# Performance work log

Measured on AMD Instinct MI355X. Metric: run time of the kernel, lower is better.

The kernel has to match this reference:

```python
import jax, jax.numpy as jnp
import numpy as np
from jax import lax

N_VAR, BATCH, N_IN, N_OUT, N_FEAT, T = 4, 32, 32, 32, 32, 256
EPS, COUPLING, GMAX, GMIN = 0.05, 0.2, 10.0, 0.01
DT, RMIN, RMAX, CMIN, CMAX = 0.1, 1e5, 1e7, 1e-7, 1e-4
ETA = np.array([0.05, 0.5, 0.3, 3.0], dtype=np.float32)  # printed-tanh activation params


def _init_theta(key, n_in, n_out):
    # xavier_uniform -> min-max normalize to [0,1], then bias-column construction as in pLayer.__init__
    a = float(np.sqrt(6.0 / (n_in + 2 + n_out)))
    t = jax.random.uniform(key, (n_in + 2, n_out), minval=-a, maxval=a)
    t = (t - t.min()) / (t.max() - t.min())
    t = t.at[-1, :].add(GMAX)
    t = t.at[-2, :].set(ETA[2] / (1.0 - ETA[2]) * (t[:-2].sum(0) + t[-1]))
    return t.astype(jnp.float32)


def setup_inputs():
    key = jax.random.key(0)
    kx, k1, k2 = jax.random.split(key, 3)
    x = jax.random.uniform(kx, (N_VAR, BATCH, N_IN, T), dtype=jnp.float32)
    theta1_ = _init_theta(k1, N_IN, N_OUT)
    theta2_ = _init_theta(k2, N_OUT * (N_FEAT + 1), N_OUT)
    # LearnableFilter init from beta_init (C_ fixed at -10, R_ is logit of normalized R)
    betas = np.linspace(0.1, 0.9, N_OUT)
    b0 = betas[:N_FEAT]
    b1 = betas[::-1][:N_FEAT]
    C_mean = 1.0 / (1.0 + np.exp(10.0)) * (CMAX - CMIN) + CMIN
    def r_(b):
        R_true = b * DT / (1.0 - b) / C_mean
        Rn = (R_true - RMIN) / (RMAX - RMIN)
        return np.log(Rn / (1.0 - Rn))
    Rlf_ = jnp.asarray(np.broadcast_to(np.stack([r_(b0), r_(b1)], -1), (N_OUT, N_FEAT, 2)).copy(), dtype=jnp.float32)
    Clf_ = jnp.full((N_OUT, N_FEAT, 2), -10.0, dtype=jnp.float32)
    return {"x": x, "theta1_": theta1_, "theta2_": theta2_, "Rlf_": Rlf_, "Clf_": Clf_}


def _theta_eff(theta_):
    # clamp + magnitude pruning with straight-through estimator
    t = jnp.clip(theta_, -GMAX, GMAX)
    t = jnp.where(jnp.abs(t) < GMIN, 0.0, t)
    return lax.stop_gradient(t) + theta_ - lax.stop_gradient(theta_)


def _pmac(a, theta_, key):
    # a: [N,B,Cin,T] -> [N,B,Cout,T]; printed MAC with sign-split weights and ideal inverter INV(a)=-a
    th = _theta_eff(theta_)
    noise = (jax.random.uniform(key, (N_VAR,) + th.shape) * 2.0 - 1.0) * EPS + 1.0
    thn = th[None] * noise  # [N,M,O]
    W = jnp.abs(thn) / (jnp.sum(jnp.abs(thn), axis=1, keepdims=True) + 1e-10)
    pos = (thn >= 0).astype(a.dtype)
    neg = 1.0 - pos
    ar = jnp.swapaxes(a, 2, 3)  # [N,B,T,Cin]
    ones = jnp.ones(ar.shape[:-1] + (1,), a.dtype)
    a_ext = jnp.concatenate([ar, ones, jnp.zeros_like(ones)], axis=-1)  # [N,B,T,M]
    a_neg = (-a_ext).at[..., -1].set(0.0)  # INV(a_ext) with last column zeroed
    z = jnp.einsum('nbtm,nmo->nbto', a_ext, W * pos) + jnp.einsum('nbtm,nmo->nbto', a_neg, W * neg)
    act = ETA[0] + ETA[1] * jnp.tanh((z - ETA[2]) * ETA[3])
    return jnp.swapaxes(act, 2, 3)


def _filter_bank(x, R_, C_, key):
    # x: [K,N,B,T]; first-order leaky integrator with fresh per-step R/C/mu noise, random init state
    K, N, B, Tt = x.shape
    Rt = jax.nn.sigmoid(R_) * (RMAX - RMIN) + RMIN  # [K]
    Ct = jax.nn.sigmoid(C_) * (CMAX - CMIN) + CMIN
    kR, kC, kmu, k0 = jax.random.split(key, 4)
    nR = (jax.random.uniform(kR, (Tt, K, N, 1)) * 2.0 - 1.0) * EPS + 1.0
    nC = (jax.random.uniform(kC, (Tt, K, N, 1)) * 2.0 - 1.0) * EPS + 1.0
    mu = jax.random.uniform(kmu, (Tt, K, N, 1)) * COUPLING + 1.0
    RC = mu * (Rt[None, :, None, None] * nR) * (Ct[None, :, None, None] * nC)
    beta = RC / (RC + DT)  # [T,K,N,1]
    s0 = jax.random.uniform(k0, (K, N, B))  # random_state=True
    xs = jnp.moveaxis(x, 3, 0)  # [T,K,N,B]
    def step(s, inp):
        x_t, b_t = inp
        return b_t * s + (1.0 - b_t) * x_t, s  # emit pre-update state (torch keeps init, drops last)
    _, outs = lax.scan(step, s0, (xs, beta))
    return jnp.moveaxis(outs, 0, 3)  # [K,N,B,T]


def reference(x, theta1_, theta2_, Rlf_, Clf_):
    key = jax.random.key(42)
    k1, k2, k3, k4 = jax.random.split(key, 4)
    a1 = _pmac(x, theta1_, k1)  # [N,B,C,T]
    N, B, C, Tt = a1.shape
    F = N_FEAT
    K = C * F
    xc = jnp.transpose(a1, (2, 0, 1, 3))  # [C,N,B,T]
    xk = jnp.broadcast_to(xc[:, None], (C, F, N, B, Tt)).reshape(K, N, B, Tt)
    y = _filter_bank(xk, Rlf_[..., 0].reshape(K), Clf_[..., 0].reshape(K), k2)
    y = _filter_bank(y, Rlf_[..., 1].reshape(K), Clf_[..., 1].reshape(K), k3)
    y = y.reshape(C, F, N, B, Tt)
    feats = jnp.concatenate([xc[:, None], y], axis=1)  # [C,F+1,N,B,T]
    h = jnp.transpose(feats, (2, 3, 0, 1, 4)).reshape(N, B, C * (F + 1), Tt)
    return _pmac(h, theta2_, k4)  # [N,B,N_out,T]
```

## Files before the change

kernel.cpp:

```cpp
#include <hip/hip_runtime.h>
#include <stdint.h>

#define C_RMIN 100000.0f
#define C_RMAX 10000000.0f
#define C_CMIN 1e-07f
#define C_CMAX 1e-04f
#define C_DT   0.1f
#define C_EPS  0.05f
#define C_COUP 0.2f

typedef __attribute__((ext_vector_type(8))) short bf16x8;
typedef __attribute__((ext_vector_type(4))) float floatx4;

__host__ __device__ inline void tf2x32(uint32_t k0, uint32_t k1,
                                       uint32_t& x0, uint32_t& x1) {
  uint32_t ks2 = k0 ^ k1 ^ 0x1BD11BDAu;
  uint32_t a = x0 + k0, b = x1 + k1;
#define TFR(r) a += b; b = (b << (r)) | (b >> (32 - (r))); b ^= a;
  TFR(13) TFR(15) TFR(26) TFR(6)
  a += k1;  b += ks2 + 1u;
  TFR(17) TFR(29) TFR(16) TFR(24)
  a += ks2; b += k0 + 2u;
  TFR(13) TFR(15) TFR(26) TFR(6)
  a += k0;  b += k1 + 3u;
  TFR(17) TFR(29) TFR(16) TFR(24)
  a += k1;  b += ks2 + 4u;
  TFR(13) TFR(15) TFR(26) TFR(6)
  a += ks2; b += k0 + 5u;
#undef TFR
  x0 = a; x1 = b;
}

__device__ inline float unif01(uint32_t k0, uint32_t k1, uint32_t e) {
  uint32_t x0 = 0u, x1 = e;
  tf2x32(k0, k1, x0, x1);
  uint32_t bits = x0 ^ x1;
  return __uint_as_float((bits >> 9) | 0x3F800000u) - 1.0f;
}

__device__ inline float theta_eff(float t) {
  t = fminf(fmaxf(t, -10.0f), 10.0f);
  return (fabsf(t) < 0.01f) ? 0.0f : t;
}

__device__ inline float sigmoidf(float x) { return 1.0f / (1.0f + expf(-x)); }

__device__ inline float noise_mul(float u) { return (u * 2.0f - 1.0f) * C_EPS + 1.0f; }

__global__ __launch_bounds__(256) void prep_kernel(
    const float* __restrict__ Rlf, const float* __restrict__ Clf,
    const float* __restrict__ theta1, const float* __restrict__ theta2,
    const float* __restrict__ x,
    float* __restrict__ beta12, float* __restrict__ a1,
    float* __restrict__ denom2p,
    uint32_t k1a, uint32_t k1b, uint32_t k4a, uint32_t k4b,
    uint32_t kR1a, uint32_t kR1b, uint32_t kC1a, uint32_t kC1b,
    uint32_t kM1a, uint32_t kM1b,
    uint32_t kR2a, uint32_t kR2b, uint32_t kC2a, uint32_t kC2b,
    uint32_t kM2a, uint32_t kM2b) {
  __shared__ float red[256];
  __shared__ float vsm[34 * 32];
  __shared__ float S1s[33 * 32];
  __shared__ float xs[32][256];
  int bid = blockIdx.x;
  int tid = threadIdx.x;
  if (bid < 32) {
    int n = bid >> 3, p = bid & 7;
    int o = tid & 31;
    int jc = tid >> 5;
    int j0 = p * 8 + jc;
    float part = 0.0f;
    for (int j = j0; j < 1058; j += 64) {
      float t = theta_eff(theta2[j * 32 + o]);
      float u = unif01(k4a, k4b, (uint32_t)((n * 1058 + j) * 32 + o));
      part += fabsf(t * noise_mul(u));
    }
    red[jc * 32 + o] = part;
    __syncthreads();
    if (jc == 0) {
      float s = 0.0f;
      for (int q = 0; q < 8; ++q) s += red[q * 32 + o];
      denom2p[(n * 8 + p) * 32 + o] = s;
    }
  } else if (bid < 160) {
    int blk = bid - 32;
    int n = blk >> 5, b = blk & 31;
    int o = tid & 31, mq = tid >> 5;
    float dp = 0.0f;
    for (int m = mq; m < 34; m += 8) {
      float t = theta_eff(theta1[m * 32 + o]);
      float v = t * noise_mul(unif01(k1a, k1b, (uint32_t)((n * 34 + m) * 32 + o)));
      vsm[m * 32 + o] = v;
      dp += fabsf(v);
    }
    red[mq * 32 + o] = dp;
    const float* xp = x + (size_t)((n * 32 + b) * 32) * 256;
    __syncthreads();
    for (int idx = tid; idx < 33 * 32; idx += 256) {
      int oo = idx & 31;
      float den = 1e-10f;
#pragma unroll
      for (int q = 0; q < 8; ++q) den += red[q * 32 + oo];
      S1s[idx] = vsm[idx] / den;
    }
    for (int m = 0; m < 32; ++m) xs[m][tid] = xp[m * 256 + tid];
    __syncthreads();
    float* ap = a1 + (size_t)((n * 32 + b) * 32) * 256;
    int t = tid;
    for (int oo = 0; oo < 32; ++oo) {
      float z = S1s[32 * 32 + oo];
#pragma unroll
      for (int m = 0; m < 32; ++m) z += xs[m][t] * S1s[m * 32 + oo];
      ap[oo * 256 + t] = 0.05f + 0.5f * tanhf((z - 0.3f) * 3.0f);
    }
  } else {
    int u = (bid - 160) * 256 + tid;
    int k = u & 1023;
    int tc = (u >> 10) & 31;
    int n = u >> 15;
    float Rt1 = sigmoidf(Rlf[k * 2 + 0]) * (C_RMAX - C_RMIN) + C_RMIN;
    float Ct1 = sigmoidf(Clf[k * 2 + 0]) * (C_CMAX - C_CMIN) + C_CMIN;
    float Rt2 = sigmoidf(Rlf[k * 2 + 1]) * (C_RMAX - C_RMIN) + C_RMIN;
    float Ct2 = sigmoidf(Clf[k * 2 + 1]) * (C_CMAX - C_CMIN) + C_CMIN;
#pragma unroll
    for (int it = 0; it < 8; ++it) {
      int t = tc * 8 + it;
      uint32_t e = (uint32_t)((t * 1024 + k) * 4 + n);
      float nR1 = noise_mul(unif01(kR1a, kR1b, e));
      float nC1 = noise_mul(unif01(kC1a, kC1b, e));
      float mu1 = unif01(kM1a, kM1b, e) * C_COUP + 1.0f;
      float rc1 = mu1 * (Rt1 * nR1) * (Ct1 * nC1);
      float nR2 = noise_mul(unif01(kR2a, kR2b, e));
      float nC2 = noise_mul(unif01(kC2a, kC2b, e));
      float mu2 = unif01(kM2a, kM2b, e) * C_COUP + 1.0f;
      float rc2 = mu2 * (Rt2 * nR2) * (Ct2 * nC2);
      float2 bb = { rc1 / (rc1 + C_DT), rc2 / (rc2 + C_DT) };
      *(float2*)&beta12[(size_t)(((n * 256 + t) * 1024) + k) * 2] = bb;
    }
  }
}

#define YP 264
#define YPLANE (16 * YP)

__global__ __launch_bounds__(320) void fk6_kernel(
    const float* __restrict__ a1, const float* __restrict__ theta2,
    const float* __restrict__ denom2p,
    const float* __restrict__ beta12, float* __restrict__ zpart,
    uint32_t k01a, uint32_t k01b, uint32_t k02a, uint32_t k02b,
    uint32_t k4a, uint32_t k4b) {
  int bid = blockIdx.x;
  int qr = bid & 3;
  int nb = bid >> 2;
  int n = nb >> 5, b = nb & 31;
  int tid = threadIdx.x;

  __shared__ __align__(16) uint8_t smem[50176];
  uint16_t* yh = (uint16_t*)smem;
  uint16_t* yl = (uint16_t*)(smem + 16896);
  short*    wf = (short*)(smem + 33792);
  __shared__ float sden[32];

  const float* a1nb = a1 + (size_t)nb * 8192;
  const float* bp = beta12 + ((size_t)n * 262144 + qr * 256) * 2;
  float* zout = zpart + (size_t)bid * 8192;

  if (tid < 32) {
    float d = 1e-10f;
#pragma unroll
    for (int q = 0; q < 8; ++q) d += denom2p[(n * 8 + q) * 32 + tid];
    sden[tid] = d;
  }
  __syncthreads();

  float s1 = 0.0f, s2 = 0.0f;
  int cc = 0;

  if (tid < 256) {
    int k = qr * 256 + tid;
    uint32_t e0 = (uint32_t)((k * 4 + n) * 32 + b);
    s1 = unif01(k01a, k01b, e0);
    s2 = unif01(k02a, k02b, e0);
    cc = k >> 5;
    for (int it = 0; it < 32; ++it) {
      int widx = it * 256 + tid;
      int j = widx & 7;
      int lane_ = (widx >> 3) & 63;
      int ot = (widx >> 9) & 1;
      int ks = widx >> 10;
      int sub = ((lane_ >> 4) << 3) + j;
      int jrow = (qr * 8 + ks) * 33 + 1 + sub;
      int oo = ot * 16 + (lane_ & 15);
      float th = theta_eff(theta2[jrow * 32 + oo]);
      float u = unif01(k4a, k4b, (uint32_t)((n * 1058 + jrow) * 32 + oo));
      float w = th * noise_mul(u) / sden[oo];
      uint32_t wb = __float_as_uint(w);
      uint32_t hi = (wb + 0x7FFFu + ((wb >> 16) & 1u)) >> 16;
      wf[(ks * 2 + ot) * 512 + lane_ * 8 + j] = (short)(uint16_t)hi;
    }
  }
  __syncthreads();

  for (int c = 0; c <= 16; ++c) {
    if (tid < 256) {
      if (c < 16) {
        uint16_t* yhb = yh + (c & 1) * YPLANE;
        uint16_t* ylb = yl + (c & 1) * YPLANE;
        int t0 = c * 16;
#pragma unroll
        for (int it = 0; it < 16; ++it) {
          int t = t0 + it;
          uint32_t sb = __float_as_uint(s2);
          uint32_t hi = sb >> 16;
          float fhi = __uint_as_float(sb & 0xFFFF0000u);
          uint32_t lo = __float_as_uint(s2 - fhi) >> 16;
          yhb[it * YP + tid] = (uint16_t)hi;
          ylb[it * YP + tid] = (uint16_t)lo;
          float2 bb = *(const float2*)&bp[(size_t)(t * 1024 + tid) * 2];
          float xv = a1nb[cc * 256 + t];
          s2 = bb.y * s2 + (1.0f - bb.y) * s1;
          s1 = bb.x * s1 + (1.0f - bb.x) * xv;
        }
      }
    } else if (c >= 1) {
      int lane = tid - 256;
      int tc = lane & 15, q = lane >> 4;
      const uint16_t* yhr = yh + ((c - 1) & 1) * YPLANE + tc * YP + q * 8;
      const uint16_t* ylr = yl + ((c - 1) & 1) * YPLANE + tc * YP + q * 8;
      floatx4 acc0a = {0,0,0,0}, acc0b = {0,0,0,0};
      floatx4 acc1a = {0,0,0,0}, acc1b = {0,0,0,0};
#pragma unroll
      for (int ks = 0; ks < 8; ++ks) {
        bf16x8 ah = *(const bf16x8*)(yhr + ks * 32);
        bf16x8 al = *(const bf16x8*)(ylr + ks * 32);
        bf16x8 bh0 = *(const bf16x8*)&wf[(ks * 2 + 0) * 512 + lane * 8];
        bf16x8 bh1 = *(const bf16x8*)&wf[(ks * 2 + 1) * 512 + lane * 8];
        if (ks & 1) {
          acc0b = __builtin_amdgcn_mfma_f32_16x16x32_bf16(ah, bh0, acc0b, 0, 0, 0);
          acc0b = __builtin_amdgcn_mfma_f32_16x16x32_bf16(al, bh0, acc0b, 0, 0, 0);
          acc1b = __builtin_amdgcn_mfma_f32_16x16x32_bf16(ah, bh1, acc1b, 0, 0, 0);
          acc1b = __builtin_amdgcn_mfma_f32_16x16x32_bf16(al, bh1, acc1b, 0, 0, 0);
        } else {
          acc0a = __builtin_amdgcn_mfma_f32_16x16x32_bf16(ah, bh0, acc0a, 0, 0, 0);
          acc0a = __builtin_amdgcn_mfma_f32_16x16x32_bf16(al, bh0, acc0a, 0, 0, 0);
          acc1a = __builtin_amdgcn_mfma_f32_16x16x32_bf16(ah, bh1, acc1a, 0, 0, 0);
          acc1a = __builtin_amdgcn_mfma_f32_16x16x32_bf16(al, bh1, acc1a, 0, 0, 0);
        }
      }
      int t0 = (c - 1) * 16;
      floatx4 r0 = acc0a + acc0b;
      floatx4 r1 = acc1a + acc1b;
      *(floatx4*)&zout[tc * 256 + t0 + q * 4] = r0;
      *(floatx4*)&zout[(16 + tc) * 256 + t0 + q * 4] = r1;
    }
    __syncthreads();
  }
}

__global__ __launch_bounds__(256) void cb2_kernel(
    const float* __restrict__ a1, const float* __restrict__ theta2,
    const float* __restrict__ denom2p,
    const float* __restrict__ zpart, float* __restrict__ out,
    uint32_t k4a, uint32_t k4b) {
  int nb = blockIdx.x;
  int n = nb >> 5;
  int t = threadIdx.x;
  __shared__ float xs[32][256];
  __shared__ float wd[33 * 32];
  __shared__ float sden[32];
  if (t < 32) {
    float d = 1e-10f;
#pragma unroll
    for (int q = 0; q < 8; ++q) d += denom2p[(n * 8 + q) * 32 + t];
    sden[t] = d;
  }
  const float* a1nb = a1 + (size_t)nb * 8192;
  for (int c = 0; c < 32; ++c) xs[c][t] = a1nb[c * 256 + t];
  __syncthreads();
  for (int idx = t; idx < 33 * 32; idx += 256) {
    int r = idx >> 5, oo = idx & 31;
    int j = (r < 32) ? r * 33 : 1056;
    float th = theta_eff(theta2[j * 32 + oo]);
    float u = unif01(k4a, k4b, (uint32_t)((n * 1058 + j) * 32 + oo));
    wd[idx] = th * noise_mul(u) / sden[oo];
  }
  __syncthreads();
  const float* zp = zpart + (size_t)nb * 4 * 8192;
  float* op = out + (size_t)nb * 8192;
  for (int o = 0; o < 32; ++o) {
    float z = wd[32 * 32 + o];
#pragma unroll
    for (int c = 0; c < 32; ++c) z += xs[c][t] * wd[c * 32 + o];
    z += zp[o * 256 + t] + zp[8192 + o * 256 + t] +
         zp[16384 + o * 256 + t] + zp[24576 + o * 256 + t];
    op[o * 256 + t] = 0.05f + 0.5f * tanhf((z - 0.3f) * 3.0f);
  }
}

struct KeyPair { uint32_t a, b; };

static inline void split4_host(KeyPair key, KeyPair out[4]) {
  for (uint32_t i = 0; i < 4; ++i) {
    uint32_t x0 = 0u, x1 = i;
    tf2x32(key.a, key.b, x0, x1);
    out[i] = {x0, x1};
  }
}

extern "C" void kernel_launch(void* const* d_in, const int* in_sizes, int n_in,
                              void* d_out, int out_size, void* d_ws, size_t ws_size,
                              hipStream_t stream) {
  const float* x   = (const float*)d_in[0];
  const float* th1 = (const float*)d_in[1];
  const float* th2 = (const float*)d_in[2];
  const float* Rlf = (const float*)d_in[3];
  const float* Clf = (const float*)d_in[4];
  float* out = (float*)d_out;
  float* ws = (float*)d_ws;

  float* den2p  = ws;
  float* a1     = ws + 1024;
  float* beta12 = ws + 1049600;
  float* zpart  = ws + 3146752;

  KeyPair root{0u, 42u};
  KeyPair kk[4];  split4_host(root, kk);
  KeyPair f1[4];  split4_host(kk[1], f1);
  KeyPair f2[4];  split4_host(kk[2], f2);

  prep_kernel<<<dim3(672), dim3(256), 0, stream>>>(
      Rlf, Clf, th1, th2, x, beta12, a1, den2p,
      kk[0].a, kk[0].b, kk[3].a, kk[3].b,
      f1[0].a, f1[0].b, f1[1].a, f1[1].b, f1[2].a, f1[2].b,
      f2[0].a, f2[0].b, f2[1].a, f2[1].b, f2[2].a, f2[2].b);
  fk6_kernel<<<dim3(512), dim3(320), 0, stream>>>(
      a1, th2, den2p, beta12, zpart,
      f1[3].a, f1[3].b, f2[3].a, f2[3].b, kk[3].a, kk[3].b);
  cb2_kernel<<<dim3(128), dim3(256), 0, stream>>>(
      a1, th2, den2p, zpart, out, kk[3].a, kk[3].b);
}
```

Baseline: 142.8 us.

## Split filter-bank kernel into 8 channel groups per batch and register-accumulate first MAC

The filter/MFMA kernel now splits the 1024 filter channels into 8 groups of 128 instead of 4 groups of 256, using 1024 blocks of 192 threads instead of 512 blocks of 320. Each block carries half the sequential scan work and half the MFMA K-depth, with smaller LDS buffers, and the block ordering is changed so blocks sharing the same beta slice run near each other. The intent is to shorten the serial recurrence critical path per block and raise occupancy. The cost is that the final combine kernel must now sum 8 partial outputs instead of 4, doubling the partial-sum traffic. Separately, the first printed MAC in the prep kernel now keeps all 32 outputs in registers and reads x directly instead of staging it through a 32 KB shared-memory tile.

```diff
diff --git a/kernel.cpp b/kernel.cpp
--- a/kernel.cpp
+++ b/kernel.cpp
@@ -61,7 +61,6 @@
   __shared__ float red[256];
   __shared__ float vsm[34 * 32];
   __shared__ float S1s[33 * 32];
-  __shared__ float xs[32][256];
   int bid = blockIdx.x;
   int tid = threadIdx.x;
   if (bid < 32) {
@@ -94,7 +93,6 @@
       dp += fabsf(v);
     }
     red[mq * 32 + o] = dp;
-    const float* xp = x + (size_t)((n * 32 + b) * 32) * 256;
     __syncthreads();
     for (int idx = tid; idx < 33 * 32; idx += 256) {
       int oo = idx & 31;
@@ -103,16 +101,20 @@
       for (int q = 0; q < 8; ++q) den += red[q * 32 + oo];
       S1s[idx] = vsm[idx] / den;
     }
-    for (int m = 0; m < 32; ++m) xs[m][tid] = xp[m * 256 + tid];
     __syncthreads();
+    const float* xp = x + (size_t)((n * 32 + b) * 32) * 256;
+    float acc[32];
+#pragma unroll
+    for (int oo = 0; oo < 32; ++oo) acc[oo] = S1s[32 * 32 + oo];
+    for (int m = 0; m < 32; ++m) {
+      float xm = xp[m * 256 + tid];
+#pragma unroll
+      for (int oo = 0; oo < 32; ++oo) acc[oo] += xm * S1s[m * 32 + oo];
+    }
     float* ap = a1 + (size_t)((n * 32 + b) * 32) * 256;
-    int t = tid;
-    for (int oo = 0; oo < 32; ++oo) {
-      float z = S1s[32 * 32 + oo];
-#pragma unroll
-      for (int m = 0; m < 32; ++m) z += xs[m][t] * S1s[m * 32 + oo];
-      ap[oo * 256 + t] = 0.05f + 0.5f * tanhf((z - 0.3f) * 3.0f);
-    }
+#pragma unroll
+    for (int oo = 0; oo < 32; ++oo)
+      ap[oo * 256 + tid] = 0.05f + 0.5f * tanhf((acc[oo] - 0.3f) * 3.0f);
   } else {
     int u = (bid - 160) * 256 + tid;
     int k = u & 1023;
@@ -140,29 +142,29 @@
   }
 }
 
-#define YP 264
+#define YP 136
 #define YPLANE (16 * YP)
 
-__global__ __launch_bounds__(320) void fk6_kernel(
+__global__ __launch_bounds__(192) void fk7_kernel(
     const float* __restrict__ a1, const float* __restrict__ theta2,
     const float* __restrict__ denom2p,
     const float* __restrict__ beta12, float* __restrict__ zpart,
     uint32_t k01a, uint32_t k01b, uint32_t k02a, uint32_t k02b,
     uint32_t k4a, uint32_t k4b) {
   int bid = blockIdx.x;
-  int qr = bid & 3;
-  int nb = bid >> 2;
-  int n = nb >> 5, b = nb & 31;
+  int g = bid & 31;
+  int b = bid >> 5;
+  int n = g >> 3, e = g & 7;
+  int nb = n * 32 + b;
   int tid = threadIdx.x;
 
-  __shared__ __align__(16) uint8_t smem[50176];
-  uint16_t* yh = (uint16_t*)smem;
-  uint16_t* yl = (uint16_t*)(smem + 16896);
-  short*    wf = (short*)(smem + 33792);
+  __shared__ __align__(16) uint16_t yh[2 * YPLANE];
+  __shared__ __align__(16) uint16_t yl[2 * YPLANE];
+  __shared__ __align__(16) short wf[8 * 512];
   __shared__ float sden[32];
 
   const float* a1nb = a1 + (size_t)nb * 8192;
-  const float* bp = beta12 + ((size_t)n * 262144 + qr * 256) * 2;
+  const float* bp = beta12 + (size_t)n * 524288 + e * 256;
   float* zout = zpart + (size_t)bid * 8192;
 
   if (tid < 32) {
@@ -176,20 +178,15 @@
   float s1 = 0.0f, s2 = 0.0f;
   int cc = 0;
 
-  if (tid < 256) {
-    int k = qr * 256 + tid;
-    uint32_t e0 = (uint32_t)((k * 4 + n) * 32 + b);
-    s1 = unif01(k01a, k01b, e0);
-    s2 = unif01(k02a, k02b, e0);
-    cc = k >> 5;
-    for (int it = 0; it < 32; ++it) {
-      int widx = it * 256 + tid;
+  for (int it = 0; it < 22; ++it) {
+    int widx = it * 192 + tid;
+    if (widx < 4096) {
       int j = widx & 7;
       int lane_ = (widx >> 3) & 63;
       int ot = (widx >> 9) & 1;
       int ks = widx >> 10;
       int sub = ((lane_ >> 4) << 3) + j;
-      int jrow = (qr * 8 + ks) * 33 + 1 + sub;
+      int jrow = (e * 4 + ks) * 33 + 1 + sub;
       int oo = ot * 16 + (lane_ & 15);
       float th = theta_eff(theta2[jrow * 32 + oo]);
       float u = unif01(k4a, k4b, (uint32_t)((n * 1058 + jrow) * 32 + oo));
@@ -199,10 +196,17 @@
       wf[(ks * 2 + ot) * 512 + lane_ * 8 + j] = (short)(uint16_t)hi;
     }
   }
+  if (tid < 128) {
+    int k = e * 128 + tid;
+    uint32_t e0 = (uint32_t)((k * 4 + n) * 32 + b);
+    s1 = unif01(k01a, k01b, e0);
+    s2 = unif01(k02a, k02b, e0);
+    cc = k >> 5;
+  }
   __syncthreads();
 
   for (int c = 0; c <= 16; ++c) {
-    if (tid < 256) {
+    if (tid < 128) {
       if (c < 16) {
         uint16_t* yhb = yh + (c & 1) * YPLANE;
         uint16_t* ylb = yl + (c & 1) * YPLANE;
@@ -216,21 +220,21 @@
           uint32_t lo = __float_as_uint(s2 - fhi) >> 16;
           yhb[it * YP + tid] = (uint16_t)hi;
           ylb[it * YP + tid] = (uint16_t)lo;
-          float2 bb = *(const float2*)&bp[(size_t)(t * 1024 + tid) * 2];
+          float2 bb = *(const float2*)&bp[(size_t)t * 2048 + tid * 2];
           float xv = a1nb[cc * 256 + t];
           s2 = bb.y * s2 + (1.0f - bb.y) * s1;
           s1 = bb.x * s1 + (1.0f - bb.x) * xv;
         }
       }
     } else if (c >= 1) {
-      int lane = tid - 256;
+      int lane = tid - 128;
       int tc = lane & 15, q = lane >> 4;
       const uint16_t* yhr = yh + ((c - 1) & 1) * YPLANE + tc * YP + q * 8;
       const uint16_t* ylr = yl + ((c - 1) & 1) * YPLANE + tc * YP + q * 8;
       floatx4 acc0a = {0,0,0,0}, acc0b = {0,0,0,0};
       floatx4 acc1a = {0,0,0,0}, acc1b = {0,0,0,0};
 #pragma unroll
-      for (int ks = 0; ks < 8; ++ks) {
+      for (int ks = 0; ks < 4; ++ks) {
         bf16x8 ah = *(const bf16x8*)(yhr + ks * 32);
         bf16x8 al = *(const bf16x8*)(ylr + ks * 32);
         bf16x8 bh0 = *(const bf16x8*)&wf[(ks * 2 + 0) * 512 + lane * 8];
@@ -257,13 +261,13 @@
   }
 }
 
-__global__ __launch_bounds__(256) void cb2_kernel(
+__global__ __launch_bounds__(256) void cb3_kernel(
     const float* __restrict__ a1, const float* __restrict__ theta2,
     const float* __restrict__ denom2p,
     const float* __restrict__ zpart, float* __restrict__ out,
     uint32_t k4a, uint32_t k4b) {
   int nb = blockIdx.x;
-  int n = nb >> 5;
+  int n = nb >> 5, b = nb & 31;
   int t = threadIdx.x;
   __shared__ float xs[32][256];
   __shared__ float wd[33 * 32];
@@ -285,14 +289,14 @@
     wd[idx] = th * noise_mul(u) / sden[oo];
   }
   __syncthreads();
-  const float* zp = zpart + (size_t)nb * 4 * 8192;
+  const float* zp = zpart + (size_t)(b * 32 + n * 8) * 8192;
   float* op = out + (size_t)nb * 8192;
   for (int o = 0; o < 32; ++o) {
     float z = wd[32 * 32 + o];
 #pragma unroll
     for (int c = 0; c < 32; ++c) z += xs[c][t] * wd[c * 32 + o];
-    z += zp[o * 256 + t] + zp[8192 + o * 256 + t] +
-         zp[16384 + o * 256 + t] + zp[24576 + o * 256 + t];
+#pragma unroll
+    for (int e = 0; e < 8; ++e) z += zp[e * 8192 + o * 256 + t];
     op[o * 256 + t] = 0.05f + 0.5f * tanhf((z - 0.3f) * 3.0f);
   }
 }
@@ -333,9 +337,9 @@
       kk[0].a, kk[0].b, kk[3].a, kk[3].b,
       f1[0].a, f1[0].b, f1[1].a, f1[1].b, f1[2].a, f1[2].b,
       f2[0].a, f2[0].b, f2[1].a, f2[1].b, f2[2].a, f2[2].b);
-  fk6_kernel<<<dim3(512), dim3(320), 0, stream>>>(
+  fk7_kernel<<<dim3(1024), dim3(192), 0, stream>>>(
       a1, th2, den2p, beta12, zpart,
       f1[3].a, f1[3].b, f2[3].a, f2[3].b, kk[3].a, kk[3].b);
-  cb2_kernel<<<dim3(128), dim3(256), 0, stream>>>(
+  cb3_kernel<<<dim3(128), dim3(256), 0, stream>>>(
       a1, th2, den2p, zpart, out, kk[3].a, kk[3].b);
 }
```

New measurement: 147.3 us. 3.2% more time.
